# Optimization experiments

Measured on AMD Instinct MI355X. Metric: run time of the kernel, lower is better.

## Reference

```python
import jax, jax.numpy as jnp
import numpy as np

FEATURE_SIZE = 1_000_000
EMB = 64
BATCH = 16384
ONEHOT = 26
MULTIHOT = 2
MH_LEN = 20
DENSE = 13
NN_IN = EMB * (ONEHOT + MULTIHOT) + DENSE  # 1805
UNITS = [1024, 512, 1]


def setup_inputs() -> dict:
    key = jax.random.key(0)
    ks = jax.random.split(key, 12)
    glorot = lambda k, shape: jax.random.normal(k, shape, jnp.float32) * np.sqrt(2.0 / (shape[0] + shape[-1])).astype(np.float32)
    return {
        "dense": jax.random.normal(ks[0], (BATCH, DENSE), jnp.float32),
        "onehot": jax.random.randint(ks[1], (BATCH, ONEHOT), 0, FEATURE_SIZE),
        "multihot": jax.random.randint(ks[2], (BATCH, MULTIHOT, MH_LEN), 0, FEATURE_SIZE),
        "fm_w": glorot(ks[3], (FEATURE_SIZE, 1)),
        "fm_emb": glorot(ks[4], (FEATURE_SIZE, EMB)),
        "w0": glorot(ks[5], (NN_IN, UNITS[0])),
        "b0": jnp.zeros((1,), jnp.float32),
        "w1": glorot(ks[6], (UNITS[0], UNITS[1])),
        "b1": jnp.zeros((1,), jnp.float32),
        "w2": glorot(ks[7], (UNITS[1], UNITS[2])),
        "b2": jnp.zeros((1,), jnp.float32),
    }


def reference(dense, onehot, multihot, fm_w, fm_emb, w0, b0, w1, b1, w2, b2):
    B = dense.shape[0]
    # Embedding gathers
    onehot_emb = fm_emb[onehot]                       # (B, 26, E)
    multihot_emb = fm_emb[multihot].mean(axis=2)      # (B, 2, L, E) -> (B, 2, E) mean combiner
    cat_emb = jnp.concatenate([onehot_emb, multihot_emb], axis=1)  # (B, 28, E)
    # FM 1st order (only onehot, as in original code)
    fm_1st = jnp.sum(fm_w[onehot], axis=1)            # (B, 1)
    # FM 2nd order: 0.5 * ((sum v)^2 - sum v^2)
    s = jnp.sum(cat_emb, axis=1)                      # (B, E)
    fm_2nd = 0.5 * (jnp.square(s) - jnp.sum(jnp.square(cat_emb), axis=1))
    fm_2nd = jnp.sum(fm_2nd, axis=1, keepdims=True)   # (B, 1)
    # Deep part (ReLU on every layer, incl. last, as in original)
    nn = jnp.concatenate([cat_emb.reshape(B, -1), dense], axis=1)  # (B, 1805)
    for w, b in ((w0, b0), (w1, b1), (w2, b2)):
        nn = jax.nn.relu(nn @ w + b)
    return jax.nn.sigmoid(fm_1st + fm_2nd + nn)       # (B, 1)
```

## Files before the change

### kernel.cpp

```cpp
#include <hip/hip_runtime.h>
#include <hip/hip_bf16.h>
#include <math.h>

typedef __attribute__((ext_vector_type(8))) short bf16x8;
typedef __attribute__((ext_vector_type(4))) float f32x4;

typedef void __attribute__((address_space(1))) gvoid_t;
typedef void __attribute__((address_space(3))) lvoid_t;

#define KP0   1856
#define NB    16384
#define OFF_X    0u
#define OFF_H0   60817408u
#define OFF_W0T  94371840u
#define OFF_W1T  98172928u
#define OFF_FM   99221504u

#define VMCNT(n) asm volatile("s_waitcnt vmcnt(" #n ")" ::: "memory")
#define LGKM0()  asm volatile("s_waitcnt lgkmcnt(0)" ::: "memory")
#define SBAR0()  __builtin_amdgcn_sched_barrier(0)

__device__ __forceinline__ float bf2f(short s) {
    return __uint_as_float(((unsigned)(unsigned short)s) << 16);
}

__device__ __forceinline__ void load_lds16(const void* g, void* l) {
    __builtin_amdgcn_global_load_lds(
        (gvoid_t*)(uintptr_t)g,
        (lvoid_t*)(unsigned)(uintptr_t)l,
        16, 0, 0);
}

__device__ __forceinline__ void transpose_tile(const float* __restrict__ W,
                                               __hip_bfloat16* __restrict__ WT,
                                               int K, int N, int KP, int k0, int n0,
                                               float (*tile)[33], int tid) {
    const int tx = tid & 31, ty = tid >> 5;
    #pragma unroll
    for (int i = 0; i < 32; i += 8) {
        int k = k0 + ty + i;
        tile[ty + i][tx] = (k < K) ? W[(size_t)k * N + (n0 + tx)] : 0.f;
    }
    __syncthreads();
    #pragma unroll
    for (int i = 0; i < 32; i += 8) {
        int n = n0 + ty + i, k = k0 + tx;
        WT[(size_t)n * KP + k] = __float2bfloat16(tile[tx][ty + i]);
    }
}

__global__ __launch_bounds__(256) void prep(const float* __restrict__ dense,
                                            const int* __restrict__ onehot,
                                            const int* __restrict__ multihot,
                                            const float* __restrict__ fm_w,
                                            const float* __restrict__ fm_emb,
                                            const float* __restrict__ w0,
                                            const float* __restrict__ w1,
                                            __hip_bfloat16* __restrict__ X,
                                            float* __restrict__ FM,
                                            __hip_bfloat16* __restrict__ W0T,
                                            __hip_bfloat16* __restrict__ W1T) {
    __shared__ float tile[32][33];
    const int b = blockIdx.x, tid = threadIdx.x;
    if (b >= 4096) {
        if (b < 4096 + 1856) {
            int bb = b - 4096;
            transpose_tile(w0, W0T, 1805, 1024, KP0, (bb % 58) * 32, (bb / 58) * 32, tile, tid);
        } else {
            int bb = b - 5952;
            transpose_tile(w1, W1T, 1024, 512, 1024, (bb % 32) * 32, (bb / 32) * 32, tile, tid);
        }
        return;
    }
    const int wv = tid >> 6, lane = tid & 63;
    const int row = b * 4 + wv;
    const int oh = (lane < 26) ? onehot[row * 26 + lane] : 0;
    const int mh = (lane < 40) ? multihot[row * 40 + lane] : 0;
    const float fm1 = (lane < 26) ? fm_w[oh] : 0.f;
    __hip_bfloat16* Xr = X + (size_t)row * KP0;
    float s = 0.f, sq = 0.f;
    for (int f = 0; f < 26; ++f) {
        int idx = __shfl(oh, f);
        float v = fm_emb[(size_t)idx * 64 + lane];
        s += v; sq += v * v;
        Xr[f * 64 + lane] = __float2bfloat16(v);
    }
    #pragma unroll
    for (int h = 0; h < 2; ++h) {
        float a = 0.f;
        for (int l = 0; l < 20; ++l) {
            int idx = __shfl(mh, h * 20 + l);
            a += fm_emb[(size_t)idx * 64 + lane];
        }
        float v = a * (1.f / 20.f);
        s += v; sq += v * v;
        Xr[(26 + h) * 64 + lane] = __float2bfloat16(v);
    }
    float red = 0.5f * (s * s - sq) + fm1;
    #pragma unroll
    for (int off = 32; off; off >>= 1) red += __shfl_xor(red, off);
    if (lane == 0) FM[row] = red;
    float dv = (lane < 13) ? dense[row * 13 + lane] : 0.f;
    Xr[1792 + lane] = __float2bfloat16(dv);
}

template<int NREP>
__global__ __launch_bounds__(512, 2) void gemm_pipe(const __hip_bfloat16* __restrict__ A,
                                                    const __hip_bfloat16* __restrict__ BT,
                                                    const float* __restrict__ bias,
                                                    __hip_bfloat16* __restrict__ C,
                                                    int M, int N, int K) {
    constexpr int BUFB = 32768 + NREP * 8192;
    constexpr int NBC  = NREP;
    __shared__ __align__(16) char lds[2][BUFB];

    const int tid = threadIdx.x;
    const int wv = tid >> 6, lane = tid & 63;
    const int lr = lane & 15, lg = lane >> 4;
    const int wr = wv >> 2, wc = wv & 3;

    const int bid = blockIdx.x;
    const int wg = (bid & 7) * 32 + (bid >> 3);
    const int br = wg >> 2, bc = wg & 3;

    const size_t rowBytes = (size_t)K * 2;
    const char* Ab = (const char*)A + (size_t)(br * 256) * rowBytes;
    const char* Bb = (const char*)BT + (size_t)(bc * (NREP * 64)) * rowBytes;
    const int nt = K >> 6;

    const int srcx = ((tid & 7) ^ ((tid >> 3) & 7)) << 4;
    auto stA = [&](int tt, int c) {
        int gr = c * 64 + (tid >> 3);
        load_lds16(Ab + (size_t)gr * rowBytes + (size_t)tt * 128 + srcx,
                   &lds[tt & 1][c * 8192 + wv * 1024]);
    };
    auto stB = [&](int tt, int c) {
        int gr = c * 64 + (tid >> 3);
        load_lds16(Bb + (size_t)gr * rowBytes + (size_t)tt * 128 + srcx,
                   &lds[tt & 1][32768 + c * 8192 + wv * 1024]);
    };

    f32x4 acc[8][NREP] = {};

    #pragma unroll
    for (int c = 0; c < 4; ++c) stA(0, c);
    #pragma unroll
    for (int c = 0; c < NBC; ++c) stB(0, c);
    #pragma unroll
    for (int c = 0; c < 4; ++c) stA(1, c);
    VMCNT(4);
    SBAR0();
    __builtin_amdgcn_s_barrier();

    const int xr0 = (lg ^ (lr & 7)) << 4;
    const int xr1 = ((4 + lg) ^ (lr & 7)) << 4;
    const int arow = (wr * 128 + lr) * 128;
    const int brow = 32768 + (wc * (NREP * 16) + lr) * 128;

    for (int t = 0; t < nt; ++t) {
        const char* L = &lds[t & 1][0];
        const bool sB = (t + 1 < nt), sA = (t + 2 < nt);
        bf16x8 a[4][2], a2[4][2], b01[2][2], b23[2][2];

        #pragma unroll
        for (int m = 0; m < 4; ++m) {
            a[m][0] = *(const bf16x8*)(L + arow + m * 2048 + xr0);
            a[m][1] = *(const bf16x8*)(L + arow + m * 2048 + xr1);
        }
        {
            constexpr int NLO = (NREP == 4) ? 2 : 1;
            #pragma unroll
            for (int n = 0; n < NLO; ++n) {
                b01[n][0] = *(const bf16x8*)(L + brow + n * 2048 + xr0);
                b01[n][1] = *(const bf16x8*)(L + brow + n * 2048 + xr1);
            }
        }
        if (sB) { stB(t + 1, 0); if constexpr (NREP == 4) stB(t + 1, 1); }
        SBAR0();
        __builtin_amdgcn_s_barrier();
        LGKM0();
        __builtin_amdgcn_s_setprio(1);
        #pragma unroll
        for (int m = 0; m < 4; ++m)
            #pragma unroll
            for (int n = 0; n < ((NREP == 4) ? 2 : 1); ++n)
                #pragma unroll
                for (int kk = 0; kk < 2; ++kk)
                    acc[m][n] = __builtin_amdgcn_mfma_f32_16x16x32_bf16(a[m][kk], b01[n][kk], acc[m][n], 0, 0, 0);
        __builtin_amdgcn_s_setprio(0);
        SBAR0();
        __builtin_amdgcn_s_barrier();

        #pragma unroll
        for (int m = 0; m < 4; ++m) {
            a2[m][0] = *(const bf16x8*)(L + arow + (4 + m) * 2048 + xr0);
            a2[m][1] = *(const bf16x8*)(L + arow + (4 + m) * 2048 + xr1);
        }
        if (sB) { if constexpr (NREP == 4) { stB(t + 1, 2); stB(t + 1, 3); } else stB(t + 1, 1); }
        SBAR0();
        __builtin_amdgcn_s_barrier();
        LGKM0();
        __builtin_amdgcn_s_setprio(1);
        #pragma unroll
        for (int m = 0; m < 4; ++m)
            #pragma unroll
            for (int n = 0; n < ((NREP == 4) ? 2 : 1); ++n)
                #pragma unroll
                for (int kk = 0; kk < 2; ++kk)
                    acc[4 + m][n] = __builtin_amdgcn_mfma_f32_16x16x32_bf16(a2[m][kk], b01[n][kk], acc[4 + m][n], 0, 0, 0);
        __builtin_amdgcn_s_setprio(0);
        SBAR0();
        __builtin_amdgcn_s_barrier();

        {
            constexpr int NHI = (NREP == 4) ? 2 : 1;
            constexpr int NO  = (NREP == 4) ? 2 : 1;
            #pragma unroll
            for (int n = 0; n < NHI; ++n) {
                b23[n][0] = *(const bf16x8*)(L + brow + (NO + n) * 2048 + xr0);
                b23[n][1] = *(const bf16x8*)(L + brow + (NO + n) * 2048 + xr1);
            }
        }
        if (sA) { stA(t + 2, 0); stA(t + 2, 1); }
        SBAR0();
        __builtin_amdgcn_s_barrier();
        LGKM0();
        __builtin_amdgcn_s_setprio(1);
        #pragma unroll
        for (int m = 0; m < 4; ++m)
            #pragma unroll
            for (int n = 0; n < ((NREP == 4) ? 2 : 1); ++n)
                #pragma unroll
                for (int kk = 0; kk < 2; ++kk)
                    acc[m][((NREP == 4) ? 2 : 1) + n] = __builtin_amdgcn_mfma_f32_16x16x32_bf16(a[m][kk], b23[n][kk], acc[m][((NREP == 4) ? 2 : 1) + n], 0, 0, 0);
        __builtin_amdgcn_s_setprio(0);
        SBAR0();
        __builtin_amdgcn_s_barrier();

        if (sA) { stA(t + 2, 2); stA(t + 2, 3); }
        SBAR0();
        __builtin_amdgcn_s_barrier();
        LGKM0();
        __builtin_amdgcn_s_setprio(1);
        #pragma unroll
        for (int m = 0; m < 4; ++m)
            #pragma unroll
            for (int n = 0; n < ((NREP == 4) ? 2 : 1); ++n)
                #pragma unroll
                for (int kk = 0; kk < 2; ++kk)
                    acc[4 + m][((NREP == 4) ? 2 : 1) + n] = __builtin_amdgcn_mfma_f32_16x16x32_bf16(a2[m][kk], b23[n][kk], acc[4 + m][((NREP == 4) ? 2 : 1) + n], 0, 0, 0);
        __builtin_amdgcn_s_setprio(0);
        SBAR0();
        if (sA)      VMCNT(4);
        else if (sB) VMCNT(0);
        if (sB) __builtin_amdgcn_s_barrier();
    }

    const float bv = bias[0];
    const int rowb = br * 256 + wr * 128, colb = bc * (NREP * 64) + wc * (NREP * 16);
    #pragma unroll
    for (int m = 0; m < 8; ++m)
        #pragma unroll
        for (int n = 0; n < NREP; ++n)
            #pragma unroll
            for (int r = 0; r < 4; ++r) {
                int row = rowb + m * 16 + lg * 4 + r;
                int col = colb + n * 16 + lr;
                C[(size_t)row * N + col] = __float2bfloat16(fmaxf(acc[m][n][r] + bv, 0.f));
            }
}

__global__ __launch_bounds__(256) void final_k(const __hip_bfloat16* __restrict__ H1,
                                               const float* __restrict__ w2,
                                               const float* __restrict__ b2,
                                               const float* __restrict__ FM,
                                               float* __restrict__ out) {
    const int wv = threadIdx.x >> 6, lane = threadIdx.x & 63;
    const int row = blockIdx.x * 4 + wv;
    const bf16x8 h = *(const bf16x8*)(H1 + (size_t)row * 512 + lane * 8);
    float s = 0.f;
    #pragma unroll
    for (int j = 0; j < 8; ++j) s += bf2f(h[j]) * w2[lane * 8 + j];
    #pragma unroll
    for (int off = 32; off; off >>= 1) s += __shfl_xor(s, off);
    if (lane == 0) {
        float v = fmaxf(s + b2[0], 0.f) + FM[row];
        out[row] = 1.f / (1.f + expf(-v));
    }
}

extern "C" void kernel_launch(void* const* d_in, const int* in_sizes, int n_in,
                              void* d_out, int out_size, void* d_ws, size_t ws_size,
                              hipStream_t stream) {
    const float* dense    = (const float*)d_in[0];
    const int*   onehot   = (const int*)d_in[1];
    const int*   multihot = (const int*)d_in[2];
    const float* fm_w     = (const float*)d_in[3];
    const float* fm_emb   = (const float*)d_in[4];
    const float* w0       = (const float*)d_in[5];
    const float* b0       = (const float*)d_in[6];
    const float* w1       = (const float*)d_in[7];
    const float* b1       = (const float*)d_in[8];
    const float* w2       = (const float*)d_in[9];
    const float* b2       = (const float*)d_in[10];
    float* out = (float*)d_out;

    char* ws = (char*)d_ws;
    __hip_bfloat16* X   = (__hip_bfloat16*)(ws + OFF_X);
    __hip_bfloat16* H1  = (__hip_bfloat16*)(ws + OFF_X);
    __hip_bfloat16* H0  = (__hip_bfloat16*)(ws + OFF_H0);
    __hip_bfloat16* W0T = (__hip_bfloat16*)(ws + OFF_W0T);
    __hip_bfloat16* W1T = (__hip_bfloat16*)(ws + OFF_W1T);
    float*          FM  = (float*)(ws + OFF_FM);

    prep<<<6464, 256, 0, stream>>>(dense, onehot, multihot, fm_w, fm_emb, w0, w1,
                                   X, FM, W0T, W1T);
    gemm_pipe<4><<<256, 512, 0, stream>>>(X,  W0T, b0, H0, NB, 1024, KP0);
    gemm_pipe<2><<<256, 512, 0, stream>>>(H0, W1T, b1, H1, NB, 512, 1024);
    final_k<<<NB / 4, 256, 0, stream>>>(H1, w2, b2, FM, out);
}
```

Before: 174.1 us.

## Fuse final 512->1 layer into second GEMM epilogue via atomic row sums

The second GEMM no longer writes its bf16 activation matrix. Its epilogue now applies ReLU, multiplies by w2, reduces across lanes and atomically adds per-row partial dot products into an NN buffer that prep zeroes. A small finish kernel then applies bias, ReLU, the FM term and the sigmoid. This removes the 16 MB H1 store and its reload, at the cost of float atomics, which make the summation order nondeterministic.

```diff
diff --git a/kernel.cpp b/kernel.cpp
--- a/kernel.cpp
+++ b/kernel.cpp
@@ -15,6 +15,7 @@
 #define OFF_W0T  94371840u
 #define OFF_W1T  98172928u
 #define OFF_FM   99221504u
+#define OFF_NN   99287040u
 
 #define VMCNT(n) asm volatile("s_waitcnt vmcnt(" #n ")" ::: "memory")
 #define LGKM0()  asm volatile("s_waitcnt lgkmcnt(0)" ::: "memory")
@@ -58,6 +59,7 @@
                                             const float* __restrict__ w1,
                                             __hip_bfloat16* __restrict__ X,
                                             float* __restrict__ FM,
+                                            float* __restrict__ NN,
                                             __hip_bfloat16* __restrict__ W0T,
                                             __hip_bfloat16* __restrict__ W1T) {
     __shared__ float tile[32][33];
@@ -100,15 +102,18 @@
     #pragma unroll
     for (int off = 32; off; off >>= 1) red += __shfl_xor(red, off);
     if (lane == 0) FM[row] = red;
+    if (lane == 32) NN[row] = 0.f;
     float dv = (lane < 13) ? dense[row * 13 + lane] : 0.f;
     Xr[1792 + lane] = __float2bfloat16(dv);
 }
 
-template<int NREP>
+template<int NREP, bool FUSED>
 __global__ __launch_bounds__(512, 2) void gemm_pipe(const __hip_bfloat16* __restrict__ A,
                                                     const __hip_bfloat16* __restrict__ BT,
                                                     const float* __restrict__ bias,
                                                     __hip_bfloat16* __restrict__ C,
+                                                    const float* __restrict__ w2,
+                                                    float* __restrict__ NN,
                                                     int M, int N, int K) {
     constexpr int BUFB = 32768 + NREP * 8192;
     constexpr int NBC  = NREP;
@@ -258,35 +263,44 @@
 
     const float bv = bias[0];
     const int rowb = br * 256 + wr * 128, colb = bc * (NREP * 64) + wc * (NREP * 16);
-    #pragma unroll
-    for (int m = 0; m < 8; ++m)
-        #pragma unroll
-        for (int n = 0; n < NREP; ++n)
+    if constexpr (FUSED) {
+        float w2v[NREP];
+        #pragma unroll
+        for (int n = 0; n < NREP; ++n) w2v[n] = w2[colb + n * 16 + lr];
+        #pragma unroll
+        for (int m = 0; m < 8; ++m)
             #pragma unroll
             for (int r = 0; r < 4; ++r) {
-                int row = rowb + m * 16 + lg * 4 + r;
-                int col = colb + n * 16 + lr;
-                C[(size_t)row * N + col] = __float2bfloat16(fmaxf(acc[m][n][r] + bv, 0.f));
+                float p = 0.f;
+                #pragma unroll
+                for (int n = 0; n < NREP; ++n)
+                    p += fmaxf(acc[m][n][r] + bv, 0.f) * w2v[n];
+                #pragma unroll
+                for (int off = 8; off; off >>= 1) p += __shfl_xor(p, off);
+                if (lr == 0)
+                    atomicAdd(&NN[rowb + m * 16 + lg * 4 + r], p);
             }
-}
-
-__global__ __launch_bounds__(256) void final_k(const __hip_bfloat16* __restrict__ H1,
-                                               const float* __restrict__ w2,
-                                               const float* __restrict__ b2,
-                                               const float* __restrict__ FM,
-                                               float* __restrict__ out) {
-    const int wv = threadIdx.x >> 6, lane = threadIdx.x & 63;
-    const int row = blockIdx.x * 4 + wv;
-    const bf16x8 h = *(const bf16x8*)(H1 + (size_t)row * 512 + lane * 8);
-    float s = 0.f;
-    #pragma unroll
-    for (int j = 0; j < 8; ++j) s += bf2f(h[j]) * w2[lane * 8 + j];
-    #pragma unroll
-    for (int off = 32; off; off >>= 1) s += __shfl_xor(s, off);
-    if (lane == 0) {
-        float v = fmaxf(s + b2[0], 0.f) + FM[row];
-        out[row] = 1.f / (1.f + expf(-v));
-    }
+    } else {
+        #pragma unroll
+        for (int m = 0; m < 8; ++m)
+            #pragma unroll
+            for (int n = 0; n < NREP; ++n)
+                #pragma unroll
+                for (int r = 0; r < 4; ++r) {
+                    int row = rowb + m * 16 + lg * 4 + r;
+                    int col = colb + n * 16 + lr;
+                    C[(size_t)row * N + col] = __float2bfloat16(fmaxf(acc[m][n][r] + bv, 0.f));
+                }
+    }
+}
+
+__global__ __launch_bounds__(256) void finish_k(const float* __restrict__ NN,
+                                                const float* __restrict__ b2,
+                                                const float* __restrict__ FM,
+                                                float* __restrict__ out) {
+    const int row = blockIdx.x * 256 + threadIdx.x;
+    float v = fmaxf(NN[row] + b2[0], 0.f) + FM[row];
+    out[row] = 1.f / (1.f + expf(-v));
 }
 
 extern "C" void kernel_launch(void* const* d_in, const int* in_sizes, int n_in,
@@ -307,15 +321,17 @@
 
     char* ws = (char*)d_ws;
     __hip_bfloat16* X   = (__hip_bfloat16*)(ws + OFF_X);
-    __hip_bfloat16* H1  = (__hip_bfloat16*)(ws + OFF_X);
     __hip_bfloat16* H0  = (__hip_bfloat16*)(ws + OFF_H0);
     __hip_bfloat16* W0T = (__hip_bfloat16*)(ws + OFF_W0T);
     __hip_bfloat16* W1T = (__hip_bfloat16*)(ws + OFF_W1T);
     float*          FM  = (float*)(ws + OFF_FM);
+    float*          NN  = (float*)(ws + OFF_NN);
 
     prep<<<6464, 256, 0, stream>>>(dense, onehot, multihot, fm_w, fm_emb, w0, w1,
-                                   X, FM, W0T, W1T);
-    gemm_pipe<4><<<256, 512, 0, stream>>>(X,  W0T, b0, H0, NB, 1024, KP0);
-    gemm_pipe<2><<<256, 512, 0, stream>>>(H0, W1T, b1, H1, NB, 512, 1024);
-    final_k<<<NB / 4, 256, 0, stream>>>(H1, w2, b2, FM, out);
-}
+                                   X, FM, NN, W0T, W1T);
+    gemm_pipe<4, false><<<256, 512, 0, stream>>>(X,  W0T, b0, H0, nullptr, nullptr,
+                                                 NB, 1024, KP0);
+    gemm_pipe<2, true><<<256, 512, 0, stream>>>(H0, W1T, b1, nullptr, w2, NN,
+                                                NB, 512, 1024);
+    finish_k<<<NB / 256, 256, 0, stream>>>(NN, b2, FM, out);
+}
```

Result: faster. 170.0 us (-2.3%).
